# Kernel optimization log

Hardware: AMD Instinct MI355X
Metric: run time of the kernel (lower is better)

## Reference

```python
import jax, jax.numpy as jnp
import numpy as np

E = 1024   # embed_dim
H = 16     # num_heads
Dh = E // H
FF = 4 * E
LN_EPS = 1e-5


def _layernorm(x, g, b):
    mu = jnp.mean(x, axis=-1, keepdims=True)
    var = jnp.var(x, axis=-1, keepdims=True)
    return (x - mu) * jax.lax.rsqrt(var + LN_EPS) * g + b


def setup_inputs() -> dict:
    key = jax.random.key(0)
    ks = jax.random.split(key, 10)
    s = lambda fan_in: 1.0 / np.sqrt(fan_in)
    x = jax.random.normal(ks[0], (2, 2048, E), dtype=jnp.float32)
    Wq = jax.random.uniform(ks[1], (H, E, Dh), jnp.float32, -s(E), s(E))
    Wk = jax.random.uniform(ks[2], (H, E, Dh), jnp.float32, -s(E), s(E))
    Wproj = jax.random.uniform(ks[3], (E, E), jnp.float32, -s(E), s(E))
    bproj = jax.random.uniform(ks[4], (E,), jnp.float32, -s(E), s(E))
    ln1_g = jnp.ones((E,), jnp.float32)
    ln1_b = jnp.zeros((E,), jnp.float32)
    ln2_g = jnp.ones((E,), jnp.float32)
    ln2_b = jnp.zeros((E,), jnp.float32)
    W1 = jax.random.uniform(ks[5], (E, FF), jnp.float32, -s(E), s(E))
    b1 = jax.random.uniform(ks[6], (FF,), jnp.float32, -s(E), s(E))
    W2 = jax.random.uniform(ks[7], (FF, E), jnp.float32, -s(FF), s(FF))
    b2 = jax.random.uniform(ks[8], (E,), jnp.float32, -s(FF), s(FF))
    return dict(x=x, Wq=Wq, Wk=Wk, Wproj=Wproj, bproj=bproj,
                ln1_g=ln1_g, ln1_b=ln1_b, ln2_g=ln2_g, ln2_b=ln2_b,
                W1=W1, b1=b1, W2=W2, b2=b2)


def reference(x, Wq, Wk, Wproj, bproj, ln1_g, ln1_b, ln2_g, ln2_b, W1, b1, W2, b2):
    B, S, _ = x.shape
    # --- self-attention branch ---
    h = _layernorm(x, ln1_g, ln1_b)
    Q = jnp.einsum('bse,hed->bhsd', h, Wq)
    K = jnp.einsum('bse,hed->bhsd', h, Wk)
    # NOTE: original code uses V = key(x), so values == keys (faithful bug).
    scores = jnp.einsum('bhqd,bhkd->bhqk', Q, K) * (1.0 / np.sqrt(Dh))
    causal = jnp.tril(jnp.ones((S, S), dtype=bool))
    scores = jnp.where(causal, scores, -jnp.inf)
    attn = jax.nn.softmax(scores, axis=-1)  # dropout is identity in eval
    out = jnp.einsum('bhqk,bhkd->bhqd', attn, K)
    out = out.transpose(0, 2, 1, 3).reshape(B, S, H * Dh)
    x = x + out @ Wproj + bproj
    # --- MLP branch ---
    h2 = _layernorm(x, ln2_g, ln2_b)
    ff = jax.nn.relu(h2 @ W1 + b1) @ W2 + b2
    return x + ff
```

## Files before the change

kernel.cpp:

```cpp
#include <hip/hip_runtime.h>
#include <stdint.h>

typedef __bf16 bf16x8 __attribute__((ext_vector_type(8)));
typedef float f32x4 __attribute__((ext_vector_type(4)));
typedef float f32x16 __attribute__((ext_vector_type(16)));
typedef unsigned short u16;
typedef unsigned int u32;
typedef unsigned int u32x2 __attribute__((ext_vector_type(2)));

__device__ __forceinline__ u16 f2bf(float f) {
    u32 u = __builtin_bit_cast(u32, f);
    u = (u + 0x7fffu + ((u >> 16) & 1u)) >> 16;
    return (u16)u;
}
__device__ __forceinline__ float bf2f(u16 x) {
    return __builtin_bit_cast(float, (u32)x << 16);
}
__device__ __forceinline__ float fexp2(float x) {
#if __has_builtin(__builtin_amdgcn_exp2f)
    return __builtin_amdgcn_exp2f(x);
#else
    return exp2f(x);
#endif
}
// ... 164 lines not shown
    o.x = f2bf((v.x - mean) * rstd * g4.x + b4.x);
    o.y = f2bf((v.y - mean) * rstd * g4.y + b4.y);
    o.z = f2bf((v.z - mean) * rstd * g4.z + b4.z);
    o.w = f2bf((v.w - mean) * rstd * g4.w + b4.w);
    *reinterpret_cast<ushort4*>(out + idx * 4) = o;
}

template<int EPI, typename OT>
__global__ __launch_bounds__(256)
void gemm_bt(const u16* __restrict__ A, const u16* __restrict__ B,
             OT* __restrict__ C, const float* __restrict__ bias,
             const float* __restrict__ res, int K, int N, u16* __restrict__ ktr) {
    __shared__ u16 Al[128 * 64];
    __shared__ u16 Bl[128 * 64];
    const int t = threadIdx.x;
    const int lane = t & 63;
    const int w = t >> 6;
    const int wm = w >> 1, wn = w & 1;
    const int l15 = lane & 15, gq = lane >> 4;
    const int gx = gridDim.x;
    const int nwg = gx * gridDim.y;
    const int bid = blockIdx.y * gx + blockIdx.x;
    const int sw = ((nwg & 7) == 0) ? ((bid & 7) * (nwg >> 3) + (bid >> 3)) : bid;
    const int col0 = (sw % gx) * 128;
    const int row0 = (sw / gx) * 128;

    f32x4 acc[4][4] = {};

    const int nkb = K >> 6;
    for (int kb = 0; kb < nkb; ++kb) {
        #pragma unroll
        for (int i = 0; i < 4; ++i) {
            int slot = i * 256 + t;
            int r = slot >> 3;
            int g = (slot & 7) ^ (r & 7);
            gload16(A + (size_t)(row0 + r) * K + kb * 64 + g * 8, Al + slot * 8);
            gload16(B + (size_t)(col0 + r) * K + kb * 64 + g * 8, Bl + slot * 8);
        }
        __syncthreads();
        #pragma unroll
        for (int s = 0; s < 2; ++s) {
            bf16x8 af[4], bfr[4];
            #pragma unroll
            for (int mi = 0; mi < 4; ++mi) {
                int rl = wm * 64 + mi * 16 + l15;
                int ba = rl * 128 + ((s * 64 + gq * 16) ^ ((rl & 7) << 4));
                af[mi] = *reinterpret_cast<const bf16x8*>(reinterpret_cast<const char*>(Al) + ba);
            }
            #pragma unroll
            for (int ni = 0; ni < 4; ++ni) {
                int rl = wn * 64 + ni * 16 + l15;
                int ba = rl * 128 + ((s * 64 + gq * 16) ^ ((rl & 7) << 4));
                bfr[ni] = *reinterpret_cast<const bf16x8*>(reinterpret_cast<const char*>(Bl) + ba);
            }
            #pragma unroll
            for (int mi = 0; mi < 4; ++mi)
                #pragma unroll
                for (int ni = 0; ni < 4; ++ni)
                    acc[mi][ni] = __builtin_amdgcn_mfma_f32_16x16x32_bf16(af[mi], bfr[ni], acc[mi][ni], 0, 0, 0);
        }
        __syncthreads();
    }

    #pragma unroll
    for (int mi = 0; mi < 4; ++mi) {
        #pragma unroll
        for (int ni = 0; ni < 4; ++ni) {
            int gcol = col0 + wn * 64 + ni * 16 + l15;
            int grow0 = row0 + wm * 64 + mi * 16 + gq * 4;
            #pragma unroll
            for (int r = 0; r < 4; ++r) {
                int grow = grow0 + r;
                float v = acc[mi][ni][r];
                if constexpr (EPI == 1 || EPI == 2) v += bias[gcol];
                if constexpr (EPI == 1) v += res[(size_t)grow * N + gcol];
                if constexpr (EPI == 2) v = fmaxf(v, 0.f);
                if constexpr (sizeof(OT) == 4) C[(size_t)grow * N + gcol] = v;
                else                           C[(size_t)grow * N + gcol] = f2bf(v);
            }
        }
    }
}

#define DS_A(MH) \
  _Pragma("unroll") \
  for (int mi = 0; mi < 4; ++mi) { \
    const int rl = wm * 128 + (MH) * 64 + mi * 16 + l15; \
    const char* rp = abase + rl * 128; \
    const int sw2 = (rl & 7) << 4; \
    af[mi][0] = *reinterpret_cast<const bf16x8*>(rp + ((gq * 16) ^ sw2)); \
    af[mi][1] = *reinterpret_cast<const bf16x8*>(rp + ((64 + gq * 16) ^ sw2)); \
  }

#define DS_B(NH) \
  _Pragma("unroll") \
  for (int ni = 0; ni < 2; ++ni) { \
    const int rl = wn * 64 + (NH) * 32 + ni * 16 + l15; \
    const char* rp = bbase + rl * 128; \
    const int sw2 = (rl & 7) << 4; \
    bfr[ni][0] = *reinterpret_cast<const bf16x8*>(rp + ((gq * 16) ^ sw2)); \
    bfr[ni][1] = *reinterpret_cast<const bf16x8*>(rp + ((64 + gq * 16) ^ sw2)); \
  }

#define ST_A(HALF, KP, DB) \
  _Pragma("unroll") \
  for (int i = 0; i < 2; ++i) { \
    const int idx = i * 512 + t; const int rs = idx >> 3; const int kc = idx & 7; \
    const int row = (rs & 63) + ((rs >> 6) << 7) + (HALF) * 64; \
    gload16(Ag + (size_t)(row0 + row) * Kf + (KP) + ((kc ^ (row & 7)) << 3), (DB) + row * 64 + kc * 8); \
  }

#define ST_B(HALF, KP, DB) \
  _Pragma("unroll") \
  for (int i = 0; i < 2; ++i) { \
    const int idx = i * 512 + t; const int rs = idx >> 3; const int kc = idx & 7; \
    const int row = (rs & 31) + ((rs >> 5) << 6) + (HALF) * 32; \
    gload16(Bg + (size_t)(col0 + row) * Kf + (KP) + ((kc ^ (row & 7)) << 3), (DB) + row * 64 + kc * 8); \
  }

#define MFMA_Q(MH, NH) \
  _Pragma("unroll") \
  for (int mi = 0; mi < 4; ++mi) { \
    _Pragma("unroll") \
    for (int ni = 0; ni < 2; ++ni) { \
      acc[MH][mi][NH][ni] = __builtin_amdgcn_mfma_f32_16x16x32_bf16(af[mi][0], bfr[ni][0], acc[MH][mi][NH][ni], 0, 0, 0); \
      acc[MH][mi][NH][ni] = __builtin_amdgcn_mfma_f32_16x16x32_bf16(af[mi][1], bfr[ni][1], acc[MH][mi][NH][ni], 0, 0, 0); \
    } \
  }

#define WAITV(N) asm volatile("s_waitcnt vmcnt(" #N ")" ::: "memory")
#define BAR() __builtin_amdgcn_s_barrier()
#define PRIO1() __builtin_amdgcn_s_setprio(1)
#define PRIO0() __builtin_amdgcn_s_setprio(0)

template<int EPI, typename OT>
__global__ __launch_bounds__(512, 2)
void gemm256(const u16* __restrict__ A, const u16* __restrict__ B, OT* __restrict__ C,
             const float* __restrict__ bias, const float* __restrict__ res,
             int Kf, int KC, int N, u16* __restrict__ ktr) {
    __shared__ u16 AL[2][16384];
    __shared__ u16 BL[2][16384];
    const int t = threadIdx.x;
    const int lane = t & 63;
    const int w = t >> 6;
    const int wm = w >> 2, wn = w & 3;
    const int l15 = lane & 15, gq = lane >> 4;
    const int gx = gridDim.x;
    const int nwg = gx * gridDim.y;
    const int bid = blockIdx.y * gx + blockIdx.x;
    const int sw = ((nwg & 7) == 0) ? ((bid & 7) * (nwg >> 3) + (bid >> 3)) : bid;
    const int col0 = (sw % gx) * 256;
    const int row0 = (sw / gx) * 256;
    const int kbase = blockIdx.z * KC;
    const u16* Ag = A;
    const u16* Bg = B;

    f32x4 acc[2][4][2][2] = {};
    bf16x8 af[4][2], bfr[2][2];

    const int NT = KC >> 6;
    { u16* An = &AL[0][0]; u16* Bn = &BL[0][0];
      ST_A(0, kbase, An); ST_B(0, kbase, Bn); ST_B(1, kbase, Bn); ST_A(1, kbase, An); }
    WAITV(4);
    BAR();

    for (int tI = 0; tI < NT - 1; ++tI) {
        const int c = tI & 1;
        const char* abase = reinterpret_cast<const char*>(&AL[c][0]);
        const char* bbase = reinterpret_cast<const char*>(&BL[c][0]);
        u16* An = &AL[c ^ 1][0];
        u16* Bn = &BL[c ^ 1][0];
        const int kn = kbase + (tI + 1) * 64;
        DS_A(0); DS_B(0);
        ST_A(0, kn, An);
        WAITV(4); BAR();
        PRIO1(); MFMA_Q(0, 0); PRIO0();
        BAR();
        DS_B(1);
        ST_B(0, kn, Bn);
        WAITV(4); BAR();
        PRIO1(); MFMA_Q(0, 1); PRIO0();
        BAR();
        DS_A(1); DS_B(0);
        ST_B(1, kn, Bn);
        BAR();
        PRIO1(); MFMA_Q(1, 0); PRIO0();
        BAR();
        DS_B(1);
        ST_A(1, kn, An);
        WAITV(4); BAR();
        PRIO1(); MFMA_Q(1, 1); PRIO0();
        BAR();
    }
    {
        const int c = (NT - 1) & 1;
        const char* abase = reinterpret_cast<const char*>(&AL[c][0]);
        const char* bbase = reinterpret_cast<const char*>(&BL[c][0]);
        DS_A(0); DS_B(0);
        WAITV(2); BAR();
        PRIO1(); MFMA_Q(0, 0); PRIO0();
        BAR();
        DS_B(1);
        WAITV(0); BAR();
        PRIO1(); MFMA_Q(0, 1); PRIO0();
        BAR();
        DS_A(1); DS_B(0);
        BAR();
        PRIO1(); MFMA_Q(1, 0); PRIO0();
        BAR();
        DS_B(1);
        PRIO1(); MFMA_Q(1, 1); PRIO0();
    }

    const size_t Crow0 = (size_t)blockIdx.z * ((size_t)gridDim.y * 256);
    #pragma unroll
    for (int mh = 0; mh < 2; ++mh)
    #pragma unroll
    for (int mi = 0; mi < 4; ++mi)
    #pragma unroll
    for (int nh = 0; nh < 2; ++nh)
    #pragma unroll
    for (int ni = 0; ni < 2; ++ni) {
        const int gcol = col0 + wn * 64 + nh * 32 + ni * 16 + l15;
        const int grow0 = row0 + wm * 128 + mh * 64 + mi * 16 + gq * 4;
        f32x4 v = acc[mh][mi][nh][ni];
        if constexpr (EPI == 2) {
            const float bb = bias[gcol];
            v[0] += bb; v[1] += bb; v[2] += bb; v[3] += bb;
        }
        if constexpr (EPI == 3) {
            if (gcol < 1024) {
                const float QS = 0.18033688f;
                v[0] *= QS; v[1] *= QS; v[2] *= QS; v[3] *= QS;
            }
        }
        #pragma unroll
        for (int r = 0; r < 4; ++r) {
            const size_t o = (Crow0 + grow0 + r) * N + gcol;
            float x = v[r];
            if constexpr (EPI == 2) x = fmaxf(x, 0.f);
            if constexpr (sizeof(OT) == 4) C[o] = x;
            else                           C[o] = f2bf(x);
        }
        if constexpr (EPI == 3) {
            if (gcol >= 1024) {
                ushort4 k4;
                k4.x = f2bf(v[0]); k4.y = f2bf(v[1]); k4.z = f2bf(v[2]); k4.w = f2bf(v[3]);
                *reinterpret_cast<ushort4*>(ktr + (size_t)(gcol - 1024) * 4096 + grow0) = k4;
            }
        }
    }
}

__global__ __launch_bounds__(256)
void reduce4_kernel(const float4* __restrict__ p0, const float4* __restrict__ p1,
                    const float4* __restrict__ p2, const float4* __restrict__ p3,
                    const float4* __restrict__ xm, const float* __restrict__ b2,
                    float4* __restrict__ out) {
    const int i = blockIdx.x * 256 + threadIdx.x;
    float4 a = p0[i], b = p1[i], c = p2[i], d = p3[i], x = xm[i];
    const float4 bb = *reinterpret_cast<const float4*>(b2 + ((i & 255) << 2));
    float4 o;
    o.x = x.x + bb.x + a.x + b.x + c.x + d.x;
    o.y = x.y + bb.y + a.y + b.y + c.y + d.y;
    o.z = x.z + bb.z + a.z + b.z + c.z + d.z;
    o.w = x.w + bb.w + a.w + b.w + c.w + d.w;
    out[i] = o;
}

template<int SPLIT>
__global__ __launch_bounds__(256)
void attn_kernel(const u16* __restrict__ qk, const u16* __restrict__ ktr, u16* __restrict__ out,
                 u16* __restrict__ pO, float* __restrict__ pl) {
    __shared__ u16 Kl[2][64 * 64];
    __shared__ u16 Tl[2][64 * 64];
    const int t = threadIdx.x;
    const int lane = t & 63;
    const int w = t >> 6;
    const int l31 = lane & 31, hi = lane >> 5;
    int bh, qb, npc, cid, s0, s1;
    if constexpr (SPLIT) {
        bh = blockIdx.x & 31;
        cid = blockIdx.x >> 5;
        qb = QB2[cid];
        const int ch = CH2[cid];
        npc = CUM2[qb + 1] - CUM2[qb];
        const int nt = 2 * (qb + 1);
        s0 = ch * 4;
        s1 = min(nt, s0 + 4);
    } else {
        bh = blockIdx.x & 31;
        const int tt = blockIdx.x >> 5;
        qb = (tt < 8) ? tt : 23 - tt;
        cid = 0; npc = 1; s0 = 0; s1 = 2 * (qb + 1);
    }
    const int b = bh >> 4, h = bh & 15;
    const int q0w = qb * 128 + w * 32;
    const int q = q0w + l31;
    const int qwmax = q0w + 31;
    const u16* Qp = qk + (size_t)b * 2048 * 2048 + h * 64;
    const u16* Kp = Qp + 1024;
    const u16* Tp = ktr + (size_t)h * 64 * 4096 + (size_t)b * 2048;

    bf16x8 qf[4];
    #pragma unroll
    for (int s = 0; s < 4; ++s)
        qf[s] = *reinterpret_cast<const bf16x8*>(Qp + (size_t)q * 2048 + s * 16 + hi * 8);

    f32x16 oacc[2] = {};
    float lsum = 0.f;

    {
        #pragma unroll
        for (int i = 0; i < 2; ++i) {
            int slot = i * 256 + t;
            int r = slot >> 3;
            int g = (slot & 7) ^ (r & 7);
            gload16(Kp + (size_t)(s0 * 64 + r) * 2048 + g * 8, &Kl[0][0] + slot * 8);
            gload16(Tp + (size_t)r * 4096 + s0 * 64 + g * 8, &Tl[0][0] + slot * 8);
        }
    }

    for (int kt = s0; kt < s1; ++kt) {
        const int cur = (kt - s0) & 1;
        __syncthreads();
        if (kt + 1 < s1) {
            int k0 = (kt + 1) * 64;
            #pragma unroll
            for (int i = 0; i < 2; ++i) {
                int slot = i * 256 + t;
                int r = slot >> 3;
                int g = (slot & 7) ^ (r & 7);
                gload16(Kp + (size_t)(k0 + r) * 2048 + g * 8, &Kl[cur ^ 1][0] + slot * 8);
                gload16(Tp + (size_t)r * 4096 + k0 + g * 8, &Tl[cur ^ 1][0] + slot * 8);
            }
        }
        const int kbase = kt * 64;
        if (kbase > qwmax) continue;
        const u16* kl = &Kl[cur][0];
        const u16* tl = &Tl[cur][0];

        f32x16 st0 = {}, st1 = {};
        PRIO1();
        #pragma unroll
        for (int s = 0; s < 4; ++s) {
            {
                int r = l31;
                int col = (16 * s + 8 * hi) ^ ((r & 7) * 8);
                bf16x8 kf = *reinterpret_cast<const bf16x8*>(kl + r * 64 + col);
// ... 93 lines not shown
        }
        if (hi == 0)
            pl[g * 128 + w * 32 + l31] = lsum;
    }
}

__global__ __launch_bounds__(256)
void attn_combine(const u16* __restrict__ pO, const float* __restrict__ pl,
                  u16* __restrict__ out) {
    const int g = blockIdx.x;
    const int bh = g & 31;
    const int qb = 2 + (g >> 5);
    const int b = bh >> 4, h = bh & 15;
    const int base = bh * 72 + CUM2[qb];
    const int npc = CUM2[qb + 1] - CUM2[qb];
    const int t = threadIdx.x;
    const int q = t >> 1;
    const int dh = (t & 1) << 5;

    float L = 0.f;
    float o[32] = {};
    for (int p = 0; p < 8; ++p) {
        if (p >= npc) break;
        L += pl[(size_t)(base + p) * 128 + q];
        const u16* src = pO + ((size_t)(base + p) * 128 + q) * 64 + dh;
        #pragma unroll
        for (int j = 0; j < 8; ++j) {
            ushort4 v = *reinterpret_cast<const ushort4*>(src + j * 4);
            o[4 * j + 0] += bf2f(v.x);
            o[4 * j + 1] += bf2f(v.y);
            o[4 * j + 2] += bf2f(v.z);
            o[4 * j + 3] += bf2f(v.w);
        }
    }
    const float inv = 1.f / L;
    u16* dst = out + ((size_t)(b * 2048 + qb * 128 + q)) * 1024 + h * 64 + dh;
    #pragma unroll
    for (int j = 0; j < 8; ++j) {
        ushort4 w4;
        w4.x = f2bf(o[4 * j + 0] * inv);
        w4.y = f2bf(o[4 * j + 1] * inv);
        w4.z = f2bf(o[4 * j + 2] * inv);
        w4.w = f2bf(o[4 * j + 3] * inv);
        *reinterpret_cast<ushort4*>(dst + j * 4) = w4;
    }
}

extern "C" void kernel_launch(void* const* d_in, const int* in_sizes, int n_in,
                              void* d_out, int out_size, void* d_ws, size_t ws_size,
                              hipStream_t stream) {
    const float* x     = (const float*)d_in[0];
    const float* Wq    = (const float*)d_in[1];
    const float* Wk    = (const float*)d_in[2];
    const float* Wproj = (const float*)d_in[3];
    const float* bproj = (const float*)d_in[4];
    const float* ln1g  = (const float*)d_in[5];
    const float* ln1b  = (const float*)d_in[6];
    const float* ln2g  = (const float*)d_in[7];
    const float* ln2b  = (const float*)d_in[8];
    const float* W1    = (const float*)d_in[9];
    const float* b1    = (const float*)d_in[10];
    const float* W2    = (const float*)d_in[11];
    const float* b2    = (const float*)d_in[12];

    char* ws = (char*)d_ws;
    u16*   wqkT   = (u16*)(ws + 0);
    u16*   wprojT = (u16*)(ws + (4ull << 20));
    u16*   w1T    = (u16*)(ws + (6ull << 20));
    u16*   w2T    = (u16*)(ws + (14ull << 20));
    u16*   hbuf   = (u16*)(ws + (22ull << 20));
    float* xmid   = (float*)(ws + (30ull << 20));
    u16*   qk     = (u16*)(ws + (46ull << 20));
    u16*   ktr    = (u16*)(ws + (62ull << 20));
    u16*   attnb  = (u16*)(ws + (70ull << 20));
    u16*   ff     = (u16*)(ws + (46ull << 20));
    float* part   = (float*)(ws + (78ull << 20));
    u16*   pO16   = (u16*)(ws + (78ull << 20));
    float* pl     = (float*)(ws + (118ull << 20));
    const bool fast = ws_size >= (142ull << 20);

    prep_all<<<6912, 256, 0, stream>>>(Wq, Wk, Wproj, W1, W2,
                                       wqkT, wprojT, w1T, w2T,
                                       x, ln1g, ln1b, hbuf);
    gemm256<3, u16><<<dim3(8, 16, 1), 512, 0, stream>>>(hbuf, wqkT, qk, nullptr, nullptr, 1024, 1024, 2048, ktr);
    if (fast) {
        attn_kernel<1><<<2304, 256, 0, stream>>>(qk, ktr, attnb, pO16, pl);
        attn_combine<<<448, 256, 0, stream>>>(pO16, pl, attnb);
    } else {
        attn_kernel<0><<<512, 256, 0, stream>>>(qk, ktr, attnb, nullptr, nullptr);
    }
    if (fast) {
        gemm256<0, float><<<dim3(4, 16, 2), 512, 0, stream>>>(attnb, wprojT, part, nullptr, nullptr, 1024, 512, 1024, nullptr);
        ln2red_kernel<<<4096, 256, 0, stream>>>(
            (const float4*)part, (const float4*)(part + 4194304), (const float4*)x,
            bproj, ln2g, ln2b, (float4*)xmid, hbuf);
    } else {
        gemm_bt<1, float><<<dim3(8, 32), 256, 0, stream>>>(attnb, wprojT, xmid, bproj, x, 1024, 1024, nullptr);
        ln_kernel<<<4096, 256, 0, stream>>>(xmid, hbuf, ln2g, ln2b);
    }
    gemm256<2, u16><<<dim3(16, 16, 1), 512, 0, stream>>>(hbuf, w1T, ff, b1, nullptr, 1024, 1024, 4096, nullptr);
    if (fast) {
        gemm256<0, float><<<dim3(4, 16, 4), 512, 0, stream>>>(ff, w2T, part, nullptr, nullptr, 4096, 1024, 1024, nullptr);
        reduce4_kernel<<<4096, 256, 0, stream>>>(
            (const float4*)part, (const float4*)(part + 4194304),
            (const float4*)(part + 2 * 4194304), (const float4*)(part + 3 * 4194304),
            (const float4*)xmid, b2, (float4*)d_out);
    } else {
        gemm_bt<1, float><<<dim3(8, 32), 256, 0, stream>>>(ff, w2T, (float*)d_out, b2, xmid, 4096, 1024, nullptr);
    }
}
```

Baseline: 235.6 us.

## Add 256x128 GEMM tile kernel and halve split-K for FFN2

Adds a gemmN128 kernel with a 256x128 output tile (occupancy hint of 2 blocks per SM) and uses it for the QK projection, the output projection and the second FFN GEMM. Twice as many blocks run per GEMM, which should fill the GPU better. The FFN2 split-K drops from 4 to 2, so the partial-sum traffic shrinks and reduce4 becomes reduce2. The cost is less B-tile reuse per block and larger per-block K loops for FFN2.

```diff
diff --git a/kernel.cpp b/kernel.cpp
--- a/kernel.cpp
+++ b/kernel.cpp
@@ -416,12 +416,6 @@
             const float bb = bias[gcol];
             v[0] += bb; v[1] += bb; v[2] += bb; v[3] += bb;
         }
-        if constexpr (EPI == 3) {
-            if (gcol < 1024) {
-                const float QS = 0.18033688f;
-                v[0] *= QS; v[1] *= QS; v[2] *= QS; v[3] *= QS;
-            }
-        }
         #pragma unroll
         for (int r = 0; r < 4; ++r) {
             const size_t o = (Crow0 + grow0 + r) * N + gcol;
@@ -430,6 +424,118 @@
             if constexpr (sizeof(OT) == 4) C[o] = x;
             else                           C[o] = f2bf(x);
         }
+    }
+}
+
+#define DS_B2 \
+  _Pragma("unroll") \
+  for (int ni = 0; ni < 2; ++ni) { \
+    const int rl = wn * 32 + ni * 16 + l15; \
+    const char* rp = bbase + rl * 128; \
+    const int sw2 = (rl & 7) << 4; \
+    bfr[ni][0] = *reinterpret_cast<const bf16x8*>(rp + ((gq * 16) ^ sw2)); \
+    bfr[ni][1] = *reinterpret_cast<const bf16x8*>(rp + ((64 + gq * 16) ^ sw2)); \
+  }
+
+#define ST_B2(KP, DB) \
+  _Pragma("unroll") \
+  for (int i = 0; i < 2; ++i) { \
+    const int idx = i * 512 + t; const int rs = idx >> 3; const int kc = idx & 7; \
+    gload16(Bg + (size_t)(col0 + rs) * Kf + (KP) + ((kc ^ (rs & 7)) << 3), (DB) + rs * 64 + kc * 8); \
+  }
+
+#define MFMA_Q2(MH) \
+  _Pragma("unroll") \
+  for (int mi = 0; mi < 4; ++mi) { \
+    _Pragma("unroll") \
+    for (int ni = 0; ni < 2; ++ni) { \
+      acc[MH][mi][ni] = __builtin_amdgcn_mfma_f32_16x16x32_bf16(af[mi][0], bfr[ni][0], acc[MH][mi][ni], 0, 0, 0); \
+      acc[MH][mi][ni] = __builtin_amdgcn_mfma_f32_16x16x32_bf16(af[mi][1], bfr[ni][1], acc[MH][mi][ni], 0, 0, 0); \
+    } \
+  }
+
+template<int EPI, typename OT>
+__global__ __launch_bounds__(512, 2)
+void gemmN128(const u16* __restrict__ A, const u16* __restrict__ B, OT* __restrict__ C,
+              int Kf, int KC, int N, u16* __restrict__ ktr) {
+    __shared__ u16 AL[2][16384];
+    __shared__ u16 BL[2][8192];
+    const int t = threadIdx.x;
+    const int lane = t & 63;
+    const int w = t >> 6;
+    const int wm = w >> 2, wn = w & 3;
+    const int l15 = lane & 15, gq = lane >> 4;
+    const int gx = gridDim.x;
+    const int nwg = gx * gridDim.y;
+    const int bid = blockIdx.y * gx + blockIdx.x;
+    const int sw = ((nwg & 7) == 0) ? ((bid & 7) * (nwg >> 3) + (bid >> 3)) : bid;
+    const int col0 = (sw % gx) * 128;
+    const int row0 = (sw / gx) * 256;
+    const int kbase = blockIdx.z * KC;
+    const u16* Ag = A;
+    const u16* Bg = B;
+
+    f32x4 acc[2][4][2] = {};
+    bf16x8 af[4][2], bfr[2][2];
+
+    const int NT = KC >> 6;
+    { u16* An = &AL[0][0]; u16* Bn = &BL[0][0];
+      ST_A(0, kbase, An); ST_B2(kbase, Bn); ST_A(1, kbase, An); }
+    WAITV(0);
+    BAR();
+
+    for (int tI = 0; tI < NT - 1; ++tI) {
+        const int c = tI & 1;
+        const char* abase = reinterpret_cast<const char*>(&AL[c][0]);
+        const char* bbase = reinterpret_cast<const char*>(&BL[c][0]);
+        u16* An = &AL[c ^ 1][0];
+        u16* Bn = &BL[c ^ 1][0];
+        const int kn = kbase + (tI + 1) * 64;
+        DS_A(0); DS_B2;
+        ST_A(0, kn, An); ST_B2(kn, Bn);
+        WAITV(4); BAR();
+        PRIO1(); MFMA_Q2(0); PRIO0();
+        BAR();
+        DS_A(1);
+        ST_A(1, kn, An);
+        WAITV(2); BAR();
+        PRIO1(); MFMA_Q2(1); PRIO0();
+        BAR();
+    }
+    {
+        const int c = (NT - 1) & 1;
+        const char* abase = reinterpret_cast<const char*>(&AL[c][0]);
+        const char* bbase = reinterpret_cast<const char*>(&BL[c][0]);
+        DS_A(0); DS_B2;
+        WAITV(0); BAR();
+        PRIO1(); MFMA_Q2(0); PRIO0();
+        BAR();
+        DS_A(1);
+        PRIO1(); MFMA_Q2(1); PRIO0();
+    }
+
+    const size_t Crow0 = (size_t)blockIdx.z * ((size_t)gridDim.y * 256);
+    #pragma unroll
+    for (int mh = 0; mh < 2; ++mh)
+    #pragma unroll
+    for (int mi = 0; mi < 4; ++mi)
+    #pragma unroll
+    for (int ni = 0; ni < 2; ++ni) {
+        const int gcol = col0 + wn * 32 + ni * 16 + l15;
+        const int grow0 = row0 + wm * 128 + mh * 64 + mi * 16 + gq * 4;
+        f32x4 v = acc[mh][mi][ni];
+        if constexpr (EPI == 3) {
+            if (gcol < 1024) {
+                const float QS = 0.18033688f;
+                v[0] *= QS; v[1] *= QS; v[2] *= QS; v[3] *= QS;
+            }
+        }
+        #pragma unroll
+        for (int r = 0; r < 4; ++r) {
+            const size_t o = (Crow0 + grow0 + r) * N + gcol;
+            if constexpr (sizeof(OT) == 4) C[o] = v[r];
+            else                           C[o] = f2bf(v[r]);
+        }
         if constexpr (EPI == 3) {
             if (gcol >= 1024) {
                 ushort4 k4;
@@ -441,18 +547,17 @@
 }
 
 __global__ __launch_bounds__(256)
-void reduce4_kernel(const float4* __restrict__ p0, const float4* __restrict__ p1,
-                    const float4* __restrict__ p2, const float4* __restrict__ p3,
+void reduce2_kernel(const float4* __restrict__ p0, const float4* __restrict__ p1,
                     const float4* __restrict__ xm, const float* __restrict__ b2,
                     float4* __restrict__ out) {
     const int i = blockIdx.x * 256 + threadIdx.x;
-    float4 a = p0[i], b = p1[i], c = p2[i], d = p3[i], x = xm[i];
+    float4 a = p0[i], b = p1[i], x = xm[i];
     const float4 bb = *reinterpret_cast<const float4*>(b2 + ((i & 255) << 2));
     float4 o;
-    o.x = x.x + bb.x + a.x + b.x + c.x + d.x;
-    o.y = x.y + bb.y + a.y + b.y + c.y + d.y;
-    o.z = x.z + bb.z + a.z + b.z + c.z + d.z;
-    o.w = x.w + bb.w + a.w + b.w + c.w + d.w;
+    o.x = x.x + bb.x + a.x + b.x;
+    o.y = x.y + bb.y + a.y + b.y;
+    o.z = x.z + bb.z + a.z + b.z;
+    o.w = x.w + bb.w + a.w + b.w;
     out[i] = o;
 }
 
@@ -712,7 +817,7 @@
     prep_all<<<6912, 256, 0, stream>>>(Wq, Wk, Wproj, W1, W2,
                                        wqkT, wprojT, w1T, w2T,
                                        x, ln1g, ln1b, hbuf);
-    gemm256<3, u16><<<dim3(8, 16, 1), 512, 0, stream>>>(hbuf, wqkT, qk, nullptr, nullptr, 1024, 1024, 2048, ktr);
+    gemmN128<3, u16><<<dim3(16, 16, 1), 512, 0, stream>>>(hbuf, wqkT, qk, 1024, 1024, 2048, ktr);
     if (fast) {
         attn_kernel<1><<<2304, 256, 0, stream>>>(qk, ktr, attnb, pO16, pl);
         attn_combine<<<448, 256, 0, stream>>>(pO16, pl, attnb);
@@ -720,7 +825,7 @@
         attn_kernel<0><<<512, 256, 0, stream>>>(qk, ktr, attnb, nullptr, nullptr);
     }
     if (fast) {
-        gemm256<0, float><<<dim3(4, 16, 2), 512, 0, stream>>>(attnb, wprojT, part, nullptr, nullptr, 1024, 512, 1024, nullptr);
+        gemmN128<0, float><<<dim3(8, 16, 2), 512, 0, stream>>>(attnb, wprojT, part, 1024, 512, 1024, nullptr);
         ln2red_kernel<<<4096, 256, 0, stream>>>(
             (const float4*)part, (const float4*)(part + 4194304), (const float4*)x,
             bproj, ln2g, ln2b, (float4*)xmid, hbuf);
@@ -730,10 +835,9 @@
     }
     gemm256<2, u16><<<dim3(16, 16, 1), 512, 0, stream>>>(hbuf, w1T, ff, b1, nullptr, 1024, 1024, 4096, nullptr);
     if (fast) {
-        gemm256<0, float><<<dim3(4, 16, 4), 512, 0, stream>>>(ff, w2T, part, nullptr, nullptr, 4096, 1024, 1024, nullptr);
-        reduce4_kernel<<<4096, 256, 0, stream>>>(
+        gemmN128<0, float><<<dim3(8, 16, 2), 512, 0, stream>>>(ff, w2T, part, 4096, 2048, 1024, nullptr);
+        reduce2_kernel<<<4096, 256, 0, stream>>>(
             (const float4*)part, (const float4*)(part + 4194304),
-            (const float4*)(part + 2 * 4194304), (const float4*)(part + 3 * 4194304),
             (const float4*)xmid, b2, (float4*)d_out);
     } else {
         gemm_bt<1, float><<<dim3(8, 32), 256, 0, stream>>>(ff, w2T, (float*)d_out, b2, xmid, 4096, 1024, nullptr);
```

New measurement: 213.2 us. 9.5% less time.

## Switch GEMMs to 256x128 tiles with triple-buffered LDS and XCD-rectangular mapping

Applied to the files above, without the earlier changes.

Replaces the 256x256 double-buffered GEMM with a 256x128-tile kernel that uses three LDS stages, prefetching two k-tiles ahead, and fewer barriers per k-step. Blocks are remapped so each XCD gets a compact rectangle of output tiles, which is meant to improve L2 reuse. Grids double in tile count, and the W2 GEMM drops from split-K 4 to split-K 2 with a matching two-way reduce kernel. The trade-off is occupancy of one block per CU (launch bounds 512,1) due to larger LDS, and less B reuse per A tile.

```diff
diff --git a/kernel.cpp b/kernel.cpp
--- a/kernel.cpp
+++ b/kernel.cpp
@@ -280,16 +280,6 @@
     af[mi][1] = *reinterpret_cast<const bf16x8*>(rp + ((64 + gq * 16) ^ sw2)); \
   }
 
-#define DS_B(NH) \
-  _Pragma("unroll") \
-  for (int ni = 0; ni < 2; ++ni) { \
-    const int rl = wn * 64 + (NH) * 32 + ni * 16 + l15; \
-    const char* rp = bbase + rl * 128; \
-    const int sw2 = (rl & 7) << 4; \
-    bfr[ni][0] = *reinterpret_cast<const bf16x8*>(rp + ((gq * 16) ^ sw2)); \
-    bfr[ni][1] = *reinterpret_cast<const bf16x8*>(rp + ((64 + gq * 16) ^ sw2)); \
-  }
-
 #define ST_A(HALF, KP, DB) \
   _Pragma("unroll") \
   for (int i = 0; i < 2; ++i) { \
@@ -298,21 +288,30 @@
     gload16(Ag + (size_t)(row0 + row) * Kf + (KP) + ((kc ^ (row & 7)) << 3), (DB) + row * 64 + kc * 8); \
   }
 
-#define ST_B(HALF, KP, DB) \
+#define DS_B2 \
+  _Pragma("unroll") \
+  for (int ni = 0; ni < 2; ++ni) { \
+    const int rl = wn * 32 + ni * 16 + l15; \
+    const char* rp = bbase + rl * 128; \
+    const int sw2 = (rl & 7) << 4; \
+    bfr[ni][0] = *reinterpret_cast<const bf16x8*>(rp + ((gq * 16) ^ sw2)); \
+    bfr[ni][1] = *reinterpret_cast<const bf16x8*>(rp + ((64 + gq * 16) ^ sw2)); \
+  }
+
+#define ST_B2(KP, DB) \
   _Pragma("unroll") \
   for (int i = 0; i < 2; ++i) { \
     const int idx = i * 512 + t; const int rs = idx >> 3; const int kc = idx & 7; \
-    const int row = (rs & 31) + ((rs >> 5) << 6) + (HALF) * 32; \
-    gload16(Bg + (size_t)(col0 + row) * Kf + (KP) + ((kc ^ (row & 7)) << 3), (DB) + row * 64 + kc * 8); \
+    gload16(Bg + (size_t)(col0 + rs) * Kf + (KP) + ((kc ^ (rs & 7)) << 3), (DB) + rs * 64 + kc * 8); \
   }
 
-#define MFMA_Q(MH, NH) \
+#define MFMA_Q2(MH) \
   _Pragma("unroll") \
   for (int mi = 0; mi < 4; ++mi) { \
     _Pragma("unroll") \
     for (int ni = 0; ni < 2; ++ni) { \
-      acc[MH][mi][NH][ni] = __builtin_amdgcn_mfma_f32_16x16x32_bf16(af[mi][0], bfr[ni][0], acc[MH][mi][NH][ni], 0, 0, 0); \
-      acc[MH][mi][NH][ni] = __builtin_amdgcn_mfma_f32_16x16x32_bf16(af[mi][1], bfr[ni][1], acc[MH][mi][NH][ni], 0, 0, 0); \
+      acc[MH][mi][ni] = __builtin_amdgcn_mfma_f32_16x16x32_bf16(af[mi][0], bfr[ni][0], acc[MH][mi][ni], 0, 0, 0); \
+      acc[MH][mi][ni] = __builtin_amdgcn_mfma_f32_16x16x32_bf16(af[mi][1], bfr[ni][1], acc[MH][mi][ni], 0, 0, 0); \
     } \
   }
 
@@ -321,13 +320,31 @@
 #define PRIO1() __builtin_amdgcn_s_setprio(1)
 #define PRIO0() __builtin_amdgcn_s_setprio(0)
 
+__device__ __forceinline__ void xcd_rect(int bid, int gx, int nwg, int& colI, int& rowI) {
+    if (nwg == 256 && gx == 16) {
+        const int xcd = bid & 7, k = bid >> 3;
+        colI = (xcd & 3) * 4 + (k & 3);
+        rowI = (xcd >> 2) * 8 + (k >> 2);
+    } else if (nwg == 128 && gx == 8) {
+        const int xcd = bid & 7, k = bid >> 3;
+        colI = (xcd & 3) * 2 + (k & 1);
+        rowI = (xcd >> 2) * 8 + (k >> 1);
+    } else if (nwg == 512 && gx == 32) {
+        const int xcd = bid & 7, k = bid >> 3;
+        colI = (xcd & 3) * 8 + (k & 7);
+        rowI = (xcd >> 2) * 8 + (k >> 3);
+    } else {
+        const int sw = ((nwg & 7) == 0) ? ((bid & 7) * (nwg >> 3) + (bid >> 3)) : bid;
+        colI = sw % gx; rowI = sw / gx;
+    }
+}
+
 template<int EPI, typename OT>
-__global__ __launch_bounds__(512, 2)
-void gemm256(const u16* __restrict__ A, const u16* __restrict__ B, OT* __restrict__ C,
-             const float* __restrict__ bias, const float* __restrict__ res,
-             int Kf, int KC, int N, u16* __restrict__ ktr) {
-    __shared__ u16 AL[2][16384];
-    __shared__ u16 BL[2][16384];
+__global__ __launch_bounds__(512, 1)
+void gemmN128(const u16* __restrict__ A, const u16* __restrict__ B, OT* __restrict__ C,
+              const float* __restrict__ bias, int Kf, int KC, int N, u16* __restrict__ ktr) {
+    __shared__ u16 AL[3][16384];
+    __shared__ u16 BL[3][8192];
     const int t = threadIdx.x;
     const int lane = t & 63;
     const int w = t >> 6;
@@ -336,68 +353,60 @@
     const int gx = gridDim.x;
     const int nwg = gx * gridDim.y;
     const int bid = blockIdx.y * gx + blockIdx.x;
-    const int sw = ((nwg & 7) == 0) ? ((bid & 7) * (nwg >> 3) + (bid >> 3)) : bid;
-    const int col0 = (sw % gx) * 256;
-    const int row0 = (sw / gx) * 256;
+    int colI, rowI;
+    xcd_rect(bid, gx, nwg, colI, rowI);
+    const int col0 = colI * 128;
+    const int row0 = rowI * 256;
     const int kbase = blockIdx.z * KC;
     const u16* Ag = A;
     const u16* Bg = B;
 
-    f32x4 acc[2][4][2][2] = {};
+    f32x4 acc[2][4][2] = {};
     bf16x8 af[4][2], bfr[2][2];
 
     const int NT = KC >> 6;
-    { u16* An = &AL[0][0]; u16* Bn = &BL[0][0];
-      ST_A(0, kbase, An); ST_B(0, kbase, Bn); ST_B(1, kbase, Bn); ST_A(1, kbase, An); }
-    WAITV(4);
-    BAR();
-
-    for (int tI = 0; tI < NT - 1; ++tI) {
-        const int c = tI & 1;
-        const char* abase = reinterpret_cast<const char*>(&AL[c][0]);
-        const char* bbase = reinterpret_cast<const char*>(&BL[c][0]);
-        u16* An = &AL[c ^ 1][0];
-        u16* Bn = &BL[c ^ 1][0];
-        const int kn = kbase + (tI + 1) * 64;
-        DS_A(0); DS_B(0);
-        ST_A(0, kn, An);
-        WAITV(4); BAR();
-        PRIO1(); MFMA_Q(0, 0); PRIO0();
-        BAR();
-        DS_B(1);
-        ST_B(0, kn, Bn);
-        WAITV(4); BAR();
-        PRIO1(); MFMA_Q(0, 1); PRIO0();
-        BAR();
-        DS_A(1); DS_B(0);
-        ST_B(1, kn, Bn);
-        BAR();
-        PRIO1(); MFMA_Q(1, 0); PRIO0();
-        BAR();
-        DS_B(1);
-        ST_A(1, kn, An);
-        WAITV(4); BAR();
-        PRIO1(); MFMA_Q(1, 1); PRIO0();
-        BAR();
+    { ST_A(0, kbase, &AL[0][0]); ST_B2(kbase, &BL[0][0]); ST_A(1, kbase, &AL[0][0]);
+      const int k1 = kbase + 64;
+      ST_A(0, k1, &AL[1][0]); ST_B2(k1, &BL[1][0]); ST_A(1, k1, &AL[1][0]); }
+
+    int cur = 0, nx2 = 2;
+    for (int tI = 0; tI < NT - 2; ++tI) {
+        const char* abase = reinterpret_cast<const char*>(&AL[cur][0]);
+        const char* bbase = reinterpret_cast<const char*>(&BL[cur][0]);
+        u16* An = &AL[nx2][0];
+        u16* Bn = &BL[nx2][0];
+        const int k2 = kbase + (tI + 2) * 64;
+        WAITV(8); BAR();
+        DS_A(0); DS_B2;
+        ST_A(0, k2, An); ST_B2(k2, Bn);
+        PRIO1(); MFMA_Q2(0); PRIO0();
+        WAITV(10); BAR();
+        DS_A(1);
+        ST_A(1, k2, An);
+        PRIO1(); MFMA_Q2(1); PRIO0();
+        cur = (cur == 2) ? 0 : cur + 1;
+        nx2 = (nx2 == 2) ? 0 : nx2 + 1;
     }
     {
-        const int c = (NT - 1) & 1;
-        const char* abase = reinterpret_cast<const char*>(&AL[c][0]);
-        const char* bbase = reinterpret_cast<const char*>(&BL[c][0]);
-        DS_A(0); DS_B(0);
+        const char* abase = reinterpret_cast<const char*>(&AL[cur][0]);
+        const char* bbase = reinterpret_cast<const char*>(&BL[cur][0]);
+        WAITV(8); BAR();
+        DS_A(0); DS_B2;
+        PRIO1(); MFMA_Q2(0); PRIO0();
+        WAITV(6); BAR();
+        DS_A(1);
+        PRIO1(); MFMA_Q2(1); PRIO0();
+        cur = (cur == 2) ? 0 : cur + 1;
+    }
+    {
+        const char* abase = reinterpret_cast<const char*>(&AL[cur][0]);
+        const char* bbase = reinterpret_cast<const char*>(&BL[cur][0]);
         WAITV(2); BAR();
-        PRIO1(); MFMA_Q(0, 0); PRIO0();
-        BAR();
-        DS_B(1);
+        DS_A(0); DS_B2;
+        PRIO1(); MFMA_Q2(0); PRIO0();
         WAITV(0); BAR();
-        PRIO1(); MFMA_Q(0, 1); PRIO0();
-        BAR();
-        DS_A(1); DS_B(0);
-        BAR();
-        PRIO1(); MFMA_Q(1, 0); PRIO0();
-        BAR();
-        DS_B(1);
-        PRIO1(); MFMA_Q(1, 1); PRIO0();
+        DS_A(1);
+        PRIO1(); MFMA_Q2(1); PRIO0();
     }
 
     const size_t Crow0 = (size_t)blockIdx.z * ((size_t)gridDim.y * 256);
@@ -406,12 +415,10 @@
     #pragma unroll
     for (int mi = 0; mi < 4; ++mi)
     #pragma unroll
-    for (int nh = 0; nh < 2; ++nh)
-    #pragma unroll
     for (int ni = 0; ni < 2; ++ni) {
-        const int gcol = col0 + wn * 64 + nh * 32 + ni * 16 + l15;
+        const int gcol = col0 + wn * 32 + ni * 16 + l15;
         const int grow0 = row0 + wm * 128 + mh * 64 + mi * 16 + gq * 4;
-        f32x4 v = acc[mh][mi][nh][ni];
+        f32x4 v = acc[mh][mi][ni];
         if constexpr (EPI == 2) {
             const float bb = bias[gcol];
             v[0] += bb; v[1] += bb; v[2] += bb; v[3] += bb;
@@ -441,18 +448,17 @@
 }
 
 __global__ __launch_bounds__(256)
-void reduce4_kernel(const float4* __restrict__ p0, const float4* __restrict__ p1,
-                    const float4* __restrict__ p2, const float4* __restrict__ p3,
+void reduce2_kernel(const float4* __restrict__ p0, const float4* __restrict__ p1,
                     const float4* __restrict__ xm, const float* __restrict__ b2,
                     float4* __restrict__ out) {
     const int i = blockIdx.x * 256 + threadIdx.x;
-    float4 a = p0[i], b = p1[i], c = p2[i], d = p3[i], x = xm[i];
+    float4 a = p0[i], b = p1[i], x = xm[i];
     const float4 bb = *reinterpret_cast<const float4*>(b2 + ((i & 255) << 2));
     float4 o;
-    o.x = x.x + bb.x + a.x + b.x + c.x + d.x;
-    o.y = x.y + bb.y + a.y + b.y + c.y + d.y;
-    o.z = x.z + bb.z + a.z + b.z + c.z + d.z;
-    o.w = x.w + bb.w + a.w + b.w + c.w + d.w;
+    o.x = x.x + bb.x + a.x + b.x;
+    o.y = x.y + bb.y + a.y + b.y;
+    o.z = x.z + bb.z + a.z + b.z;
+    o.w = x.w + bb.w + a.w + b.w;
     out[i] = o;
 }
 
@@ -712,7 +718,7 @@
     prep_all<<<6912, 256, 0, stream>>>(Wq, Wk, Wproj, W1, W2,
                                        wqkT, wprojT, w1T, w2T,
                                        x, ln1g, ln1b, hbuf);
-    gemm256<3, u16><<<dim3(8, 16, 1), 512, 0, stream>>>(hbuf, wqkT, qk, nullptr, nullptr, 1024, 1024, 2048, ktr);
+    gemmN128<3, u16><<<dim3(16, 16, 1), 512, 0, stream>>>(hbuf, wqkT, qk, nullptr, 1024, 1024, 2048, ktr);
     if (fast) {
         attn_kernel<1><<<2304, 256, 0, stream>>>(qk, ktr, attnb, pO16, pl);
         attn_combine<<<448, 256, 0, stream>>>(pO16, pl, attnb);
@@ -720,7 +726,7 @@
         attn_kernel<0><<<512, 256, 0, stream>>>(qk, ktr, attnb, nullptr, nullptr);
     }
     if (fast) {
-        gemm256<0, float><<<dim3(4, 16, 2), 512, 0, stream>>>(attnb, wprojT, part, nullptr, nullptr, 1024, 512, 1024, nullptr);
+        gemmN128<0, float><<<dim3(8, 16, 2), 512, 0, stream>>>(attnb, wprojT, part, nullptr, 1024, 512, 1024, nullptr);
         ln2red_kernel<<<4096, 256, 0, stream>>>(
             (const float4*)part, (const float4*)(part + 4194304), (const float4*)x,
             bproj, ln2g, ln2b, (float4*)xmid, hbuf);
@@ -728,12 +734,11 @@
         gemm_bt<1, float><<<dim3(8, 32), 256, 0, stream>>>(attnb, wprojT, xmid, bproj, x, 1024, 1024, nullptr);
         ln_kernel<<<4096, 256, 0, stream>>>(xmid, hbuf, ln2g, ln2b);
     }
-    gemm256<2, u16><<<dim3(16, 16, 1), 512, 0, stream>>>(hbuf, w1T, ff, b1, nullptr, 1024, 1024, 4096, nullptr);
+    gemmN128<2, u16><<<dim3(32, 16, 1), 512, 0, stream>>>(hbuf, w1T, ff, b1, 1024, 1024, 4096, nullptr);
     if (fast) {
-        gemm256<0, float><<<dim3(4, 16, 4), 512, 0, stream>>>(ff, w2T, part, nullptr, nullptr, 4096, 1024, 1024, nullptr);
-        reduce4_kernel<<<4096, 256, 0, stream>>>(
+        gemmN128<0, float><<<dim3(8, 16, 2), 512, 0, stream>>>(ff, w2T, part, nullptr, 4096, 2048, 1024, nullptr);
+        reduce2_kernel<<<4096, 256, 0, stream>>>(
             (const float4*)part, (const float4*)(part + 4194304),
-            (const float4*)(part + 2 * 4194304), (const float4*)(part + 3 * 4194304),
             (const float4*)xmid, b2, (float4*)d_out);
     } else {
         gemm_bt<1, float><<<dim3(8, 32), 256, 0, stream>>>(ff, w2T, (float*)d_out, b2, xmid, 4096, 1024, nullptr);
```

New measurement: 214.2 us. 9.1% less time.

## Restructure 256-tile GEMM pipeline with deeper prefetch and XCD-rectangular tile mapping

Applied to the files above, without the earlier changes.

The GEMM main loop is rewritten to process two K-tiles per iteration, with prefetch issued further ahead: the next tile's first A half and B half are loaded before the loop starts, and waits are relaxed to vmcnt 6/8. B fragments are now double-buffered in registers, one set per N half. A new xcd_rect mapping gives each XCD a rectangular block of output tiles for the 256- and 128-workgroup grids to improve L2 reuse. The launch bound drops the two-blocks-per-SM hint, which frees registers but may reduce occupancy.

```diff
diff --git a/kernel.cpp b/kernel.cpp
--- a/kernel.cpp
+++ b/kernel.cpp
@@ -270,24 +270,24 @@
     }
 }
 
-#define DS_A(MH) \
+#define DS_A(MH, AB) \
   _Pragma("unroll") \
   for (int mi = 0; mi < 4; ++mi) { \
     const int rl = wm * 128 + (MH) * 64 + mi * 16 + l15; \
-    const char* rp = abase + rl * 128; \
+    const char* rp = reinterpret_cast<const char*>(AB) + rl * 128; \
     const int sw2 = (rl & 7) << 4; \
     af[mi][0] = *reinterpret_cast<const bf16x8*>(rp + ((gq * 16) ^ sw2)); \
     af[mi][1] = *reinterpret_cast<const bf16x8*>(rp + ((64 + gq * 16) ^ sw2)); \
   }
 
-#define DS_B(NH) \
+#define DS_B(NH, BB) \
   _Pragma("unroll") \
   for (int ni = 0; ni < 2; ++ni) { \
     const int rl = wn * 64 + (NH) * 32 + ni * 16 + l15; \
-    const char* rp = bbase + rl * 128; \
+    const char* rp = reinterpret_cast<const char*>(BB) + rl * 128; \
     const int sw2 = (rl & 7) << 4; \
-    bfr[ni][0] = *reinterpret_cast<const bf16x8*>(rp + ((gq * 16) ^ sw2)); \
-    bfr[ni][1] = *reinterpret_cast<const bf16x8*>(rp + ((64 + gq * 16) ^ sw2)); \
+    bfr[NH][ni][0] = *reinterpret_cast<const bf16x8*>(rp + ((gq * 16) ^ sw2)); \
+    bfr[NH][ni][1] = *reinterpret_cast<const bf16x8*>(rp + ((64 + gq * 16) ^ sw2)); \
   }
 
 #define ST_A(HALF, KP, DB) \
@@ -298,11 +298,11 @@
     gload16(Ag + (size_t)(row0 + row) * Kf + (KP) + ((kc ^ (row & 7)) << 3), (DB) + row * 64 + kc * 8); \
   }
 
-#define ST_B(HALF, KP, DB) \
+#define ST_BN(NH, KP, DB) \
   _Pragma("unroll") \
   for (int i = 0; i < 2; ++i) { \
     const int idx = i * 512 + t; const int rs = idx >> 3; const int kc = idx & 7; \
-    const int row = (rs & 31) + ((rs >> 5) << 6) + (HALF) * 32; \
+    const int row = (rs & 31) + ((rs >> 5) << 6) + (NH) * 32; \
     gload16(Bg + (size_t)(col0 + row) * Kf + (KP) + ((kc ^ (row & 7)) << 3), (DB) + row * 64 + kc * 8); \
   }
 
@@ -311,8 +311,8 @@
   for (int mi = 0; mi < 4; ++mi) { \
     _Pragma("unroll") \
     for (int ni = 0; ni < 2; ++ni) { \
-      acc[MH][mi][NH][ni] = __builtin_amdgcn_mfma_f32_16x16x32_bf16(af[mi][0], bfr[ni][0], acc[MH][mi][NH][ni], 0, 0, 0); \
-      acc[MH][mi][NH][ni] = __builtin_amdgcn_mfma_f32_16x16x32_bf16(af[mi][1], bfr[ni][1], acc[MH][mi][NH][ni], 0, 0, 0); \
+      acc[MH][mi][NH][ni] = __builtin_amdgcn_mfma_f32_16x16x32_bf16(af[mi][0], bfr[NH][ni][0], acc[MH][mi][NH][ni], 0, 0, 0); \
+      acc[MH][mi][NH][ni] = __builtin_amdgcn_mfma_f32_16x16x32_bf16(af[mi][1], bfr[NH][ni][1], acc[MH][mi][NH][ni], 0, 0, 0); \
     } \
   }
 
@@ -321,11 +321,25 @@
 #define PRIO1() __builtin_amdgcn_s_setprio(1)
 #define PRIO0() __builtin_amdgcn_s_setprio(0)
 
+__device__ __forceinline__ void xcd_rect(int bid, int gx, int nwg, int& colI, int& rowI) {
+    if (nwg == 256 && gx == 16) {
+        const int xcd = bid & 7, k = bid >> 3;
+        colI = (xcd & 3) * 4 + (k & 3);
+        rowI = (xcd >> 2) * 8 + (k >> 2);
+    } else if (nwg == 128 && gx == 8) {
+        const int xcd = bid & 7, k = bid >> 3;
+        colI = (xcd & 3) * 2 + (k & 1);
+        rowI = (xcd >> 2) * 8 + (k >> 1);
+    } else {
+        const int sw = ((nwg & 7) == 0) ? ((bid & 7) * (nwg >> 3) + (bid >> 3)) : bid;
+        colI = sw % gx; rowI = sw / gx;
+    }
+}
+
 template<int EPI, typename OT>
-__global__ __launch_bounds__(512, 2)
-void gemm256(const u16* __restrict__ A, const u16* __restrict__ B, OT* __restrict__ C,
-             const float* __restrict__ bias, const float* __restrict__ res,
-             int Kf, int KC, int N, u16* __restrict__ ktr) {
+__global__ __launch_bounds__(512)
+void gemm256d(const u16* __restrict__ A, const u16* __restrict__ B, OT* __restrict__ C,
+              const float* __restrict__ bias, int Kf, int KC, int N, u16* __restrict__ ktr) {
     __shared__ u16 AL[2][16384];
     __shared__ u16 BL[2][16384];
     const int t = threadIdx.x;
@@ -336,67 +350,68 @@
     const int gx = gridDim.x;
     const int nwg = gx * gridDim.y;
     const int bid = blockIdx.y * gx + blockIdx.x;
-    const int sw = ((nwg & 7) == 0) ? ((bid & 7) * (nwg >> 3) + (bid >> 3)) : bid;
-    const int col0 = (sw % gx) * 256;
-    const int row0 = (sw / gx) * 256;
+    int colI, rowI;
+    xcd_rect(bid, gx, nwg, colI, rowI);
+    const int col0 = colI * 256;
+    const int row0 = rowI * 256;
     const int kbase = blockIdx.z * KC;
     const u16* Ag = A;
     const u16* Bg = B;
 
     f32x4 acc[2][4][2][2] = {};
-    bf16x8 af[4][2], bfr[2][2];
+    bf16x8 af[4][2];
+    bf16x8 bfr[2][2][2];
 
     const int NT = KC >> 6;
-    { u16* An = &AL[0][0]; u16* Bn = &BL[0][0];
-      ST_A(0, kbase, An); ST_B(0, kbase, Bn); ST_B(1, kbase, Bn); ST_A(1, kbase, An); }
-    WAITV(4);
-    BAR();
-
-    for (int tI = 0; tI < NT - 1; ++tI) {
-        const int c = tI & 1;
-        const char* abase = reinterpret_cast<const char*>(&AL[c][0]);
-        const char* bbase = reinterpret_cast<const char*>(&BL[c][0]);
-        u16* An = &AL[c ^ 1][0];
-        u16* Bn = &BL[c ^ 1][0];
-        const int kn = kbase + (tI + 1) * 64;
-        DS_A(0); DS_B(0);
-        ST_A(0, kn, An);
-        WAITV(4); BAR();
-        PRIO1(); MFMA_Q(0, 0); PRIO0();
-        BAR();
-        DS_B(1);
-        ST_B(0, kn, Bn);
-        WAITV(4); BAR();
-        PRIO1(); MFMA_Q(0, 1); PRIO0();
-        BAR();
-        DS_A(1); DS_B(0);
-        ST_B(1, kn, Bn);
-        BAR();
-        PRIO1(); MFMA_Q(1, 0); PRIO0();
-        BAR();
-        DS_B(1);
-        ST_A(1, kn, An);
-        WAITV(4); BAR();
-        PRIO1(); MFMA_Q(1, 1); PRIO0();
-        BAR();
+    const int NS = NT >> 1;
+
+    ST_A(0, kbase, &AL[0][0]); ST_BN(0, kbase, &BL[0][0]);
+    ST_BN(1, kbase, &BL[0][0]); ST_A(1, kbase, &AL[0][0]);
+    ST_A(0, kbase + 64, &AL[1][0]); ST_BN(0, kbase + 64, &BL[1][0]);
+    WAITV(6); BAR();
+
+    for (int s = 0; s < NS - 1; ++s) {
+        const int t0 = kbase + s * 128;
+        DS_A(0, &AL[0][0]); DS_B(0, &BL[0][0]);
+        ST_BN(1, t0 + 64, &BL[1][0]);
+        BAR(); PRIO1(); MFMA_Q(0, 0); PRIO0(); BAR();
+        DS_B(1, &BL[0][0]);
+        ST_A(1, t0 + 64, &AL[1][0]);
+        WAITV(8); BAR(); PRIO1(); MFMA_Q(0, 1); PRIO0(); BAR();
+        DS_A(1, &AL[0][0]);
+        ST_A(0, t0 + 128, &AL[0][0]);
+        BAR(); PRIO1(); MFMA_Q(1, 0); PRIO0(); BAR();
+        ST_BN(0, t0 + 128, &BL[0][0]);
+        WAITV(6); BAR(); PRIO1(); MFMA_Q(1, 1); PRIO0(); BAR();
+        DS_A(0, &AL[1][0]); DS_B(0, &BL[1][0]);
+        ST_BN(1, t0 + 128, &BL[0][0]);
+        BAR(); PRIO1(); MFMA_Q(0, 0); PRIO0(); BAR();
+        DS_B(1, &BL[1][0]);
+        ST_A(1, t0 + 128, &AL[0][0]);
+        WAITV(8); BAR(); PRIO1(); MFMA_Q(0, 1); PRIO0(); BAR();
+        DS_A(1, &AL[1][0]);
+        ST_A(0, t0 + 192, &AL[1][0]);
+        BAR(); PRIO1(); MFMA_Q(1, 0); PRIO0(); BAR();
+        ST_BN(0, t0 + 192, &BL[1][0]);
+        WAITV(6); BAR(); PRIO1(); MFMA_Q(1, 1); PRIO0(); BAR();
     }
     {
-        const int c = (NT - 1) & 1;
-        const char* abase = reinterpret_cast<const char*>(&AL[c][0]);
-        const char* bbase = reinterpret_cast<const char*>(&BL[c][0]);
-        DS_A(0); DS_B(0);
-        WAITV(2); BAR();
-        PRIO1(); MFMA_Q(0, 0); PRIO0();
-        BAR();
-        DS_B(1);
-        WAITV(0); BAR();
-        PRIO1(); MFMA_Q(0, 1); PRIO0();
-        BAR();
-        DS_A(1); DS_B(0);
-        BAR();
-        PRIO1(); MFMA_Q(1, 0); PRIO0();
-        BAR();
-        DS_B(1);
+        const int t0 = kbase + KC - 128;
+        DS_A(0, &AL[0][0]); DS_B(0, &BL[0][0]);
+        ST_BN(1, t0 + 64, &BL[1][0]);
+        BAR(); PRIO1(); MFMA_Q(0, 0); PRIO0(); BAR();
+        DS_B(1, &BL[0][0]);
+        ST_A(1, t0 + 64, &AL[1][0]);
+        WAITV(8); BAR(); PRIO1(); MFMA_Q(0, 1); PRIO0(); BAR();
+        DS_A(1, &AL[0][0]);
+        BAR(); PRIO1(); MFMA_Q(1, 0); PRIO0(); BAR();
+        WAITV(2); BAR(); PRIO1(); MFMA_Q(1, 1); PRIO0(); BAR();
+        DS_A(0, &AL[1][0]); DS_B(0, &BL[1][0]);
+        BAR(); PRIO1(); MFMA_Q(0, 0); PRIO0(); BAR();
+        DS_B(1, &BL[1][0]);
+        WAITV(0); BAR(); PRIO1(); MFMA_Q(0, 1); PRIO0(); BAR();
+        DS_A(1, &AL[1][0]);
+        BAR(); PRIO1(); MFMA_Q(1, 0); PRIO0(); BAR();
         PRIO1(); MFMA_Q(1, 1); PRIO0();
     }
 
@@ -712,7 +727,7 @@
     prep_all<<<6912, 256, 0, stream>>>(Wq, Wk, Wproj, W1, W2,
                                        wqkT, wprojT, w1T, w2T,
                                        x, ln1g, ln1b, hbuf);
-    gemm256<3, u16><<<dim3(8, 16, 1), 512, 0, stream>>>(hbuf, wqkT, qk, nullptr, nullptr, 1024, 1024, 2048, ktr);
+    gemm256d<3, u16><<<dim3(8, 16, 1), 512, 0, stream>>>(hbuf, wqkT, qk, nullptr, 1024, 1024, 2048, ktr);
     if (fast) {
         attn_kernel<1><<<2304, 256, 0, stream>>>(qk, ktr, attnb, pO16, pl);
         attn_combine<<<448, 256, 0, stream>>>(pO16, pl, attnb);
@@ -720,7 +735,7 @@
         attn_kernel<0><<<512, 256, 0, stream>>>(qk, ktr, attnb, nullptr, nullptr);
     }
     if (fast) {
-        gemm256<0, float><<<dim3(4, 16, 2), 512, 0, stream>>>(attnb, wprojT, part, nullptr, nullptr, 1024, 512, 1024, nullptr);
+        gemm256d<0, float><<<dim3(4, 16, 2), 512, 0, stream>>>(attnb, wprojT, part, nullptr, 1024, 512, 1024, nullptr);
         ln2red_kernel<<<4096, 256, 0, stream>>>(
             (const float4*)part, (const float4*)(part + 4194304), (const float4*)x,
             bproj, ln2g, ln2b, (float4*)xmid, hbuf);
@@ -728,9 +743,9 @@
         gemm_bt<1, float><<<dim3(8, 32), 256, 0, stream>>>(attnb, wprojT, xmid, bproj, x, 1024, 1024, nullptr);
         ln_kernel<<<4096, 256, 0, stream>>>(xmid, hbuf, ln2g, ln2b);
     }
-    gemm256<2, u16><<<dim3(16, 16, 1), 512, 0, stream>>>(hbuf, w1T, ff, b1, nullptr, 1024, 1024, 4096, nullptr);
+    gemm256d<2, u16><<<dim3(16, 16, 1), 512, 0, stream>>>(hbuf, w1T, ff, b1, 1024, 1024, 4096, nullptr);
     if (fast) {
-        gemm256<0, float><<<dim3(4, 16, 4), 512, 0, stream>>>(ff, w2T, part, nullptr, nullptr, 4096, 1024, 1024, nullptr);
+        gemm256d<0, float><<<dim3(4, 16, 4), 512, 0, stream>>>(ff, w2T, part, nullptr, 4096, 1024, 1024, nullptr);
         reduce4_kernel<<<4096, 256, 0, stream>>>(
             (const float4*)part, (const float4*)(part + 4194304),
             (const float4*)(part + 2 * 4194304), (const float4*)(part + 3 * 4194304),
```

Measured after the change: 237.4 us. Within noise of the previous version (+0.7%).
